# Performance work log

Measured on AMD Instinct MI355X. Metric: run time of the kernel, lower is better.

## Reference

```python
import jax, jax.numpy as jnp
import numpy as np

B, S = 16, 1024
V, D, P = 100000, 256, 8


def setup_inputs() -> dict:
    key = jax.random.key(0)
    k1, k2, k3, k4 = jax.random.split(key, 4)
    x = jax.random.randint(k1, (B, S), 0, V, dtype=jnp.int64 if jax.config.jax_enable_x64 else jnp.int32)
    emb_table = jax.random.normal(k2, (V, D), dtype=jnp.float32)
    weight = jax.random.normal(k3, (P, D, D), dtype=jnp.float32)
    partitions = jax.random.randint(k4, (V,), 0, P, dtype=jnp.int32)
    return {"x": x, "emb_table": emb_table, "weight": weight, "partitions": partitions}


def reference(x, emb_table, weight, partitions):
    P_, Dz, Dx = weight.shape
    # mask[p, x] = 1 for x < D >> p (reset_parameters halves active dim per partition)
    active = (Dx >> jnp.arange(P_))  # [P]
    mask = (jnp.arange(Dx)[None, :] < active[:, None]).astype(weight.dtype)  # [P, Dx]
    mw = weight * mask[:, None, :]  # [P, Dz, Dx], masked partition weights

    emb = emb_table[x]          # [B, S, Dx] token embeddings
    part = partitions[x]        # [B, S] partition id per token

    # Compute all P candidate outputs (small fixed P), then select per token.
    # Mathematically identical to gathering mw[part] and doing per-token matvec,
    # but avoids the huge [B,S,Dz,Dx] gathered-weight intermediate.
    all_out = jnp.einsum('bsx,pzx->bspz', emb, mw)  # [B, S, P, Dz]
    out = jnp.take_along_axis(all_out, part[..., None, None], axis=2)[..., 0, :]  # [B, S, Dz]
    return out
```

## Files before the change

kernel.cpp:

```cpp
#include <hip/hip_runtime.h>

__global__ void bucket_k(const int* __restrict__ x, const int* __restrict__ parts,
                         int* __restrict__ counts, int* __restrict__ buckets, int NT) {
    __shared__ int lcount[8];
    __shared__ int lbase[8];
    const int tid = threadIdx.x;
    if (tid < 8) lcount[tid] = 0;
    __syncthreads();

    const int i = blockIdx.x * blockDim.x + tid;
    int p = 0, lpos = 0;
    const bool valid = (i < NT);
    if (valid) {
        p = parts[x[i]];
        lpos = atomicAdd(&lcount[p], 1);
    }
    __syncthreads();
    if (tid < 8)
        lbase[tid] = lcount[tid] ? atomicAdd(&counts[tid], lcount[tid]) : 0;
    __syncthreads();
    if (valid)
        buckets[(size_t)p * NT + lbase[p] + lpos] = i;
}

#define KC 32
#define XB 32

__global__ __launch_bounds__(256)
void fge_gemm(const int* __restrict__ x,
              const float* __restrict__ emb,
              const float* __restrict__ weight,
              const int* __restrict__ counts,
              const int* __restrict__ buckets,
              float* __restrict__ out, int NT) {
    const int p = blockIdx.z;
    const int n = counts[p];
    if ((int)(blockIdx.x * 64) >= n) return;
    const int z0  = blockIdx.y * 64;
    const int K   = 256 >> p;
    const int tid = threadIdx.x;

    __shared__ __align__(16) float w_lds[256][64];
    __shared__ __align__(16) float e_lds[KC][64];
    __shared__ int vrow[64];
    __shared__ int oidx[64];

    {
        const int Kpad = (K < KC) ? KC : K;
        const int wrow = tid >> 2;
        const float* wbase = weight + ((size_t)p * 256 + (z0 + wrow)) * 256;
        for (int colb = (tid & 3) * 4; colb < Kpad; colb += 16) {
            float4 v = *(const float4*)(wbase + colb);
            float vv[4] = {v.x, v.y, v.z, v.w};
#pragma unroll
            for (int c = 0; c < 4; ++c)
                w_lds[colb + c][wrow] = (colb + c < K) ? vv[c] : 0.f;
        }
    }

    const int tz  = tid & 15;
    const int tt  = tid >> 4;
    const int t_l = tid & 63;
    const int xh  = tid >> 6;
    const int nch = (K + KC - 1) / KC;

    for (int t0 = blockIdx.x * 64; t0 < n; t0 += XB * 64) {
        const int ntile = min(64, n - t0);

        __syncthreads();
        if (tid < 64) {
            int idx = 0, row = 0;
            if (t_l < ntile) {
                idx = buckets[(size_t)p * NT + t0 + t_l];
                row = x[idx];
            }
            oidx[t_l] = idx;
            vrow[t_l] = row;
        }
        __syncthreads();

        float acc[4][4] = {};

        for (int ch = 0; ch < nch; ++ch) {
            {
                const bool tv = (t_l < ntile);
                const float* er = emb + (size_t)vrow[t_l] * 256;
                const int gxb = ch * KC + xh * 8;
                float4 a = *(const float4*)(er + gxb);
                float4 b = *(const float4*)(er + gxb + 4);
                float va[8] = {a.x, a.y, a.z, a.w, b.x, b.y, b.z, b.w};
#pragma unroll
                for (int c = 0; c < 8; ++c) {
                    int gx = gxb + c;
                    e_lds[xh * 8 + c][t_l] = (tv && gx < K) ? va[c] : 0.f;
                }
            }
            __syncthreads();

#pragma unroll
            for (int c = 0; c < KC; ++c) {
                const float4 ev = *(const float4*)&e_lds[c][tt * 4];
                const float4 wv = *(const float4*)&w_lds[ch * KC + c][tz * 4];
                const float ea[4] = {ev.x, ev.y, ev.z, ev.w};
                const float wa[4] = {wv.x, wv.y, wv.z, wv.w};
#pragma unroll
                for (int i = 0; i < 4; ++i)
#pragma unroll
                    for (int j = 0; j < 4; ++j)
                        acc[i][j] = fmaf(ea[i], wa[j], acc[i][j]);
            }
            __syncthreads();
        }

#pragma unroll
        for (int i = 0; i < 4; ++i) {
            const int t = tt * 4 + i;
            if (t < ntile) {
                float4 o = {acc[i][0], acc[i][1], acc[i][2], acc[i][3]};
                *(float4*)(out + (size_t)oidx[t] * 256 + z0 + tz * 4) = o;
            }
        }
    }
}

__global__ void naive_k(const int* __restrict__ x, const float* __restrict__ emb,
                        const float* __restrict__ w, const int* __restrict__ parts,
                        float* __restrict__ out, int D, int P) {
    const int i = blockIdx.x;
    const int tokrow = x[i];
    const int p = parts[tokrow];
    const int K = D >> p;
    const float* er = emb + (size_t)tokrow * D;
    for (int z = threadIdx.x; z < D; z += blockDim.x) {
        const float* wr = w + ((size_t)p * D + z) * D;
        float acc = 0.f;
        for (int k = 0; k < K; ++k) acc = fmaf(er[k], wr[k], acc);
        out[(size_t)i * D + z] = acc;
    }
}

extern "C" void kernel_launch(void* const* d_in, const int* in_sizes, int n_in,
                              void* d_out, int out_size, void* d_ws, size_t ws_size,
                              hipStream_t stream) {
    const int*   xi    = (const int*)d_in[0];
    const float* emb   = (const float*)d_in[1];
    const float* wgt   = (const float*)d_in[2];
    const int*   parts = (const int*)d_in[3];
    float* out = (float*)d_out;

    const int NT = in_sizes[0];
    const long long V = in_sizes[3];
    const int D = (int)(in_sizes[1] / V);
    const int P = (int)(in_sizes[2] / ((long long)D * D));
    const size_t need = 32 + (size_t)P * (size_t)NT * sizeof(int);

    if (D == 256 && P == 8 && ws_size >= need) {
        int* counts  = (int*)d_ws;
        int* buckets = (int*)((char*)d_ws + 32);
        hipMemsetAsync(counts, 0, 32, stream);
        bucket_k<<<(NT + 255) / 256, 256, 0, stream>>>(xi, parts, counts, buckets, NT);
        dim3 grid(XB, 4, 8);
        fge_gemm<<<grid, 256, 0, stream>>>(xi, emb, wgt, counts, buckets, out, NT);
    } else {
        naive_k<<<NT, 256, 0, stream>>>(xi, emb, wgt, parts, out, D, P);
    }
}
```

Before: 164.0 us.

## Cover full output width per block and stream weight chunks instead of preloading

The grouped GEMM now has each block compute all 256 output columns for a tile of 32 tokens, so the z dimension of the grid goes away. Embedding rows are gathered once per token instead of four times. Weight rows are loaded per K-chunk into a smaller LDS buffer rather than preloading a 64-column slab of the whole matrix, which cuts LDS use and may allow more resident blocks. Each thread now accumulates 4x8 values, which raises register pressure. Weight reloads per token tile also increase global or L2 traffic.

```diff
diff --git a/kernel.cpp b/kernel.cpp
--- a/kernel.cpp
+++ b/kernel.cpp
@@ -23,8 +23,9 @@
         buckets[(size_t)p * NT + lbase[p] + lpos] = i;
 }
 
+#define TT 32
 #define KC 32
-#define XB 32
+#define XB 80
 
 __global__ __launch_bounds__(256)
 void fge_gemm(const int* __restrict__ x,
@@ -33,66 +34,59 @@
               const int* __restrict__ counts,
               const int* __restrict__ buckets,
               float* __restrict__ out, int NT) {
-    const int p = blockIdx.z;
+    const int p = blockIdx.y;
     const int n = counts[p];
-    if ((int)(blockIdx.x * 64) >= n) return;
-    const int z0  = blockIdx.y * 64;
+    if ((int)(blockIdx.x * TT) >= n) return;
     const int K   = 256 >> p;
+    const int nch = (K + KC - 1) / KC;
     const int tid = threadIdx.x;
 
-    __shared__ __align__(16) float w_lds[256][64];
-    __shared__ __align__(16) float e_lds[KC][64];
-    __shared__ int vrow[64];
-    __shared__ int oidx[64];
+    __shared__ __align__(16) float e_lds[KC][TT];
+    __shared__ __align__(16) float w_lds[KC][256];
+    __shared__ int vrow[TT];
+    __shared__ int oidx[TT];
 
-    {
-        const int Kpad = (K < KC) ? KC : K;
-        const int wrow = tid >> 2;
-        const float* wbase = weight + ((size_t)p * 256 + (z0 + wrow)) * 256;
-        for (int colb = (tid & 3) * 4; colb < Kpad; colb += 16) {
-            float4 v = *(const float4*)(wbase + colb);
-            float vv[4] = {v.x, v.y, v.z, v.w};
-#pragma unroll
-            for (int c = 0; c < 4; ++c)
-                w_lds[colb + c][wrow] = (colb + c < K) ? vv[c] : 0.f;
-        }
-    }
+    const int tt  = tid & 7;
+    const int tz  = tid >> 3;
+    const int t_s = tid & 31;
+    const int xh  = tid >> 5;
 
-    const int tz  = tid & 15;
-    const int tt  = tid >> 4;
-    const int t_l = tid & 63;
-    const int xh  = tid >> 6;
-    const int nch = (K + KC - 1) / KC;
-
-    for (int t0 = blockIdx.x * 64; t0 < n; t0 += XB * 64) {
-        const int ntile = min(64, n - t0);
+    for (int t0 = blockIdx.x * TT; t0 < n; t0 += XB * TT) {
+        const int ntile = min(TT, n - t0);
 
         __syncthreads();
-        if (tid < 64) {
+        if (tid < TT) {
             int idx = 0, row = 0;
-            if (t_l < ntile) {
-                idx = buckets[(size_t)p * NT + t0 + t_l];
+            if (tid < ntile) {
+                idx = buckets[(size_t)p * NT + t0 + tid];
                 row = x[idx];
             }
-            oidx[t_l] = idx;
-            vrow[t_l] = row;
+            oidx[tid] = idx;
+            vrow[tid] = row;
         }
         __syncthreads();
 
-        float acc[4][4] = {};
+        float acc[4][8] = {};
 
         for (int ch = 0; ch < nch; ++ch) {
             {
-                const bool tv = (t_l < ntile);
-                const float* er = emb + (size_t)vrow[t_l] * 256;
-                const int gxb = ch * KC + xh * 8;
-                float4 a = *(const float4*)(er + gxb);
-                float4 b = *(const float4*)(er + gxb + 4);
-                float va[8] = {a.x, a.y, a.z, a.w, b.x, b.y, b.z, b.w};
+                const bool tv = (t_s < ntile);
+                const int gxb = ch * KC + xh * 4;
+                const float4 v = *(const float4*)(emb + (size_t)vrow[t_s] * 256 + gxb);
+                const float va[4] = {v.x, v.y, v.z, v.w};
 #pragma unroll
-                for (int c = 0; c < 8; ++c) {
-                    int gx = gxb + c;
-                    e_lds[xh * 8 + c][t_l] = (tv && gx < K) ? va[c] : 0.f;
+                for (int c = 0; c < 4; ++c)
+                    e_lds[xh * 4 + c][t_s] = (tv && (gxb + c) < K) ? va[c] : 0.f;
+            }
+            {
+                const float* wr = weight + ((size_t)p * 256 + tid) * 256 + ch * KC;
+#pragma unroll
+                for (int i = 0; i < KC / 4; ++i) {
+                    const float4 v = *(const float4*)(wr + i * 4);
+                    w_lds[i * 4 + 0][tid] = v.x;
+                    w_lds[i * 4 + 1][tid] = v.y;
+                    w_lds[i * 4 + 2][tid] = v.z;
+                    w_lds[i * 4 + 3][tid] = v.w;
                 }
             }
             __syncthreads();
@@ -100,13 +94,14 @@
 #pragma unroll
             for (int c = 0; c < KC; ++c) {
                 const float4 ev = *(const float4*)&e_lds[c][tt * 4];
-                const float4 wv = *(const float4*)&w_lds[ch * KC + c][tz * 4];
+                const float4 w0 = *(const float4*)&w_lds[c][tz * 8];
+                const float4 w1 = *(const float4*)&w_lds[c][tz * 8 + 4];
                 const float ea[4] = {ev.x, ev.y, ev.z, ev.w};
-                const float wa[4] = {wv.x, wv.y, wv.z, wv.w};
+                const float wa[8] = {w0.x, w0.y, w0.z, w0.w, w1.x, w1.y, w1.z, w1.w};
 #pragma unroll
                 for (int i = 0; i < 4; ++i)
 #pragma unroll
-                    for (int j = 0; j < 4; ++j)
+                    for (int j = 0; j < 8; ++j)
                         acc[i][j] = fmaf(ea[i], wa[j], acc[i][j]);
             }
             __syncthreads();
@@ -116,8 +111,11 @@
         for (int i = 0; i < 4; ++i) {
             const int t = tt * 4 + i;
             if (t < ntile) {
-                float4 o = {acc[i][0], acc[i][1], acc[i][2], acc[i][3]};
-                *(float4*)(out + (size_t)oidx[t] * 256 + z0 + tz * 4) = o;
+                float* op = out + (size_t)oidx[t] * 256 + tz * 8;
+                float4 o0 = {acc[i][0], acc[i][1], acc[i][2], acc[i][3]};
+                float4 o1 = {acc[i][4], acc[i][5], acc[i][6], acc[i][7]};
+                *(float4*)op = o0;
+                *(float4*)(op + 4) = o1;
             }
         }
     }
@@ -159,7 +157,7 @@
         int* buckets = (int*)((char*)d_ws + 32);
         hipMemsetAsync(counts, 0, 32, stream);
         bucket_k<<<(NT + 255) / 256, 256, 0, stream>>>(xi, parts, counts, buckets, NT);
-        dim3 grid(XB, 4, 8);
+        dim3 grid(XB, 8);
         fge_gemm<<<grid, 256, 0, stream>>>(xi, emb, wgt, counts, buckets, out, NT);
     } else {
         naive_k<<<NT, 256, 0, stream>>>(xi, emb, wgt, parts, out, D, P);
```

New measurement: 170.0 us. 3.6% more time.
